# Kernel optimization log

Hardware: AMD Instinct MI355X
Metric: run time of the kernel (lower is better)

Reference implementation:

```python
import jax, jax.numpy as jnp
import numpy as np

B, L, H, E = 8, 1024, 8, 64
S, D = 1024, 64


def fp(x):
    # power-norm with p=2: norm(x) * x^2 / norm(x^2)
    norm = jnp.sqrt(jnp.sum(x * x, axis=-1, keepdims=True))
    px = x * x  # x^p, p=2
    pnorm = jnp.sqrt(jnp.sum(px * px, axis=-1, keepdims=True))
    return norm * px / pnorm


def phi_p(x):
    return fp(jax.nn.relu(x))


def setup_inputs() -> dict:
    key = jax.random.key(0)
    kq, kk, kv = jax.random.split(key, 3)
    queries = jax.random.normal(kq, (B, L, H, E), dtype=jnp.float32)
    keys = jax.random.normal(kk, (B, S, H, E), dtype=jnp.float32)
    values = jax.random.normal(kv, (B, S, H, D), dtype=jnp.float32)
    # all-False mask: masked_fill(-inf) + fp() would NaN otherwise (see notes)
    attn_mask = jnp.zeros((B, 1, L, S), dtype=bool)
    return {"queries": queries, "keys": keys, "values": values, "attn_mask": attn_mask}


def reference(queries, keys, values, attn_mask):
    qt = phi_p(queries)              # [B,L,H,E]
    kt = phi_p(keys)                 # [B,S,H,E]
    scores = jnp.einsum('blhe,bshe->bhls', qt, kt)  # [B,H,L,S]
    scores = jnp.where(attn_mask, -jnp.inf, scores)  # mask_flag=True path
    # NB: original computes scale = 1/sqrt(E) but never applies it.
    A = jax.nn.softmax(fp(scores), axis=-1)  # dropout is identity at eval
    V = jnp.einsum('bhls,bshd->blhd', A, values)  # [B,L,H,D]
    return V
```

## Files before the change

### kernel.cpp

```cpp
#include <hip/hip_runtime.h>
#include <hip/hip_bf16.h>


#define B_ 8
#define L_ 1024
#define H_ 8
#define E_ 64
#define S_ 1024
#define D_ 64
#define BH_ 64

typedef _Float16 f16_t;
typedef _Float16 f16x8 __attribute__((ext_vector_type(8)));
typedef _Float16 f16x4v __attribute__((ext_vector_type(4)));
typedef float f32x4 __attribute__((ext_vector_type(4)));
typedef unsigned u32x4 __attribute__((ext_vector_type(4)));

#define MFMA16F(a, b, c) __builtin_amdgcn_mfma_f32_16x16x32_f16(a, b, c, 0, 0, 0)
#define GLDS16(g, l)                                                        \
  __builtin_amdgcn_global_load_lds(                                         \
      (const __attribute__((address_space(1))) void*)(g),                   \
      (__attribute__((address_space(3))) void*)(l), 16, 0, 0)

#if __has_builtin(__builtin_amdgcn_exp2f)
#define EXP2(x) __builtin_amdgcn_exp2f(x)
#else
#define EXP2(x) exp2f(x)
#endif

static __device__ __forceinline__ unsigned pkh(float a, float b) {
  return __builtin_bit_cast(unsigned, __builtin_amdgcn_cvt_pkrtz(a, b));
}

static __device__ __forceinline__ void pl32_swap(unsigned& x, unsigned& y) {
#if __has_builtin(__builtin_amdgcn_permlane32_swap)
  auto r = __builtin_amdgcn_permlane32_swap(x, y, false, false);
  x = r[0];
  y = r[1];
#else
  unsigned xs = __shfl_xor((int)x, 32, 64), ys = __shfl_xor((int)y, 32, 64);
  bool hi = (threadIdx.x & 32) != 0;
  unsigned nx = hi ? ys : x;
  unsigned ny = hi ? y : xs;
  x = nx;
  y = ny;
#endif
}

static __device__ __forceinline__ void pl16_swap(unsigned& x, unsigned& y) {
#if __has_builtin(__builtin_amdgcn_permlane16_swap)
  auto r = __builtin_amdgcn_permlane16_swap(x, y, false, false);
  x = r[0];
  y = r[1];
#else
  unsigned xs = __shfl_xor((int)x, 16, 64), ys = __shfl_xor((int)y, 16, 64);
  bool odd = (threadIdx.x & 16) != 0;
  unsigned nx = odd ? ys : x;
  unsigned ny = odd ? y : xs;
  x = nx;
  y = ny;
#endif
}

__global__ __launch_bounds__(256) void prep_kernel(
    const float* __restrict__ q, const float* __restrict__ k,
    const float* __restrict__ v, f16_t* __restrict__ qf,
    f16_t* __restrict__ kf, f16_t* __restrict__ vt) {
  __shared__ float tile[32][68];
  int bid = blockIdx.x;
  if (bid < 8192) {
    int row = bid * 16 + (threadIdx.x >> 4);
    int p = threadIdx.x & 15;
    const float* src;
    f16_t* dst;
    int r = row;
    if (r < B_ * L_ * H_) { src = q; dst = qf; }
    else { r -= B_ * L_ * H_; src = k; dst = kf; }
    int b = r >> 13;
    int l = (r >> 3) & 1023;
    int h = r & 7;
    float4 x = ((const float4*)(src + (size_t)r * 64))[p];
    float s0 = fmaxf(x.x, 0.f) * fmaxf(x.x, 0.f);
    float s1 = fmaxf(x.y, 0.f) * fmaxf(x.y, 0.f);
    float s2 = fmaxf(x.z, 0.f) * fmaxf(x.z, 0.f);
    float s3 = fmaxf(x.w, 0.f) * fmaxf(x.w, 0.f);
    float sum2 = (s0 + s1) + (s2 + s3);
    float sum4 = fmaf(s0, s0, s1 * s1) + fmaf(s2, s2, s3 * s3);
#pragma unroll
    for (int off = 1; off < 16; off <<= 1) {
      sum2 += __shfl_xor(sum2, off, 64);
      sum4 += __shfl_xor(sum4, off, 64);
    }
    float sc = (sum4 > 0.f) ? sqrtf(sum2 / sum4) : 0.f;
    f16x4v o = {(f16_t)(sc * s0), (f16_t)(sc * s1), (f16_t)(sc * s2),
                (f16_t)(sc * s3)};
    int c = p >> 1, e = (p & 1) * 4;
    int col = (((c ^ (l & 7)) << 3) | e);
    *(f16x4v*)(dst + ((size_t)(b * H_ + h) * 1024 + l) * 64 + col) = o;
  } else {
    int vb = bid - 8192;
    int bh = vb >> 5;
    int st = vb & 31;
    int b = bh >> 3, h = bh & 7;
    int t = threadIdx.x;
    int sl = t >> 3, dp = t & 7;
    const float* src =
        v + (((size_t)(b * S_ + st * 32 + sl) * H_ + h) * D_) + dp * 8;
    float4 f0 = ((const float4*)src)[0];
    float4 f1 = ((const float4*)src)[1];
    *(float4*)&tile[sl][dp * 8] = f0;
    *(float4*)&tile[sl][dp * 8 + 4] = f1;
    __syncthreads();
    int d = t >> 2, sc = t & 3;
    f16_t tmp[8];
#pragma unroll
    for (int j = 0; j < 8; ++j) tmp[j] = (f16_t)tile[sc * 8 + j][d];
    f16_t* dst =
        vt + (((size_t)bh * 32 + st) * 64 + d) * 32 + (sc ^ ((d >> 1) & 3)) * 8;
    *(uint4*)dst = *(const uint4*)tmp;
  }
}

__global__ __launch_bounds__(512, 4) void attn_kernel(
    const f16_t* __restrict__ qf, const f16_t* __restrict__ kf,
    const f16_t* __restrict__ vt, float* __restrict__ out) {
  __shared__ __align__(16) f16_t k_t[2][2][2048];
  __shared__ __align__(16) f16_t v_t[2][2][2048];
  __shared__ __align__(16) float mrg[4][64][34];

  int bh = blockIdx.x & 63;
  int qb = blockIdx.x >> 6;
  int b = bh >> 3, h = bh & 7;
  int tid = threadIdx.x;
  int wave = tid >> 6, lane = tid & 63;
  int wv = wave & 3, sh = wave >> 2;
  int g = lane >> 4, n = lane & 15;

  const f16_t* qf_b = qf + ((size_t)bh * L_ + qb * 128) * 64;
  const f16_t* kf_b = kf + (size_t)bh * S_ * 64 + (size_t)sh * 16 * 2048;
  const f16_t* vt_b = vt + (size_t)bh * 32 * 2048 + (size_t)sh * 16 * 2048;

  int arow = wv * 32 + n;
  int qoff0 = arow * 64 + ((g ^ (n & 7)) << 3);
  int qoff1 = qoff0 + 16 * 64;
  f16x8 qa0_0 = *(const f16x8*)(qf_b + qoff0);
  f16x8 qa1_0 = *(const f16x8*)(qf_b + (qoff0 ^ 32));
  f16x8 qa0_1 = *(const f16x8*)(qf_b + qoff1);
  f16x8 qa1_1 = *(const f16x8*)(qf_b + (qoff1 ^ 32));

  int koff = n * 64 + ((g ^ (n & 7)) << 3);
  int voff = n * 32 + ((g ^ ((n >> 1) & 3)) << 3);
  int so = (tid & 255) * 8;

  const f32x4 fzero = {0.f, 0.f, 0.f, 0.f};
  f32x4 acc2_0 = fzero, acc4_0 = fzero, mx_0 = fzero;
  f32x4 acc2_1 = fzero, acc4_1 = fzero, mx_1 = fzero;

  GLDS16(kf_b + so, &k_t[sh][0][so]);
  for (int t = 0; t < 16; ++t) {
    __syncthreads();
    if (t < 15)
      GLDS16(kf_b + (t + 1) * 2048 + so, &k_t[sh][(t + 1) & 1][so]);
    const f16_t* kt = k_t[sh][t & 1];
    f16x8 b00 = *(const f16x8*)(kt + koff);
    f16x8 b01 = *(const f16x8*)(kt + (koff ^ 32));
    f16x8 b10 = *(const f16x8*)(kt + koff + 1024);
    f16x8 b11 = *(const f16x8*)(kt + (koff ^ 32) + 1024);
    f32x4 sc0_0 = MFMA16F(b00, qa0_0, fzero);
    sc0_0 = MFMA16F(b01, qa1_0, sc0_0);
    f32x4 sc1_0 = MFMA16F(b10, qa0_0, fzero);
    sc1_0 = MFMA16F(b11, qa1_0, sc1_0);
    f32x4 sc0_1 = MFMA16F(b00, qa0_1, fzero);
    sc0_1 = MFMA16F(b01, qa1_1, sc0_1);
    f32x4 sc1_1 = MFMA16F(b10, qa0_1, fzero);
    sc1_1 = MFMA16F(b11, qa1_1, sc1_1);
    f32x4 t0 = sc0_0 * sc0_0, t1 = sc1_0 * sc1_0;
    acc2_0 += t0 + t1;
    acc4_0 += t0 * t0;
    acc4_0 += t1 * t1;
    mx_0 = __builtin_elementwise_max(mx_0, __builtin_elementwise_max(t0, t1));
    f32x4 u0 = sc0_1 * sc0_1, u1 = sc1_1 * sc1_1;
    acc2_1 += u0 + u1;
    acc4_1 += u0 * u0;
    acc4_1 += u1 * u1;
    mx_1 = __builtin_elementwise_max(mx_1, __builtin_elementwise_max(u0, u1));
  }
  GLDS16(kf_b + so, &k_t[sh][0][so]);
  GLDS16(vt_b + so, &v_t[sh][0][so]);

  float a2_0 = (acc2_0[0] + acc2_0[1]) + (acc2_0[2] + acc2_0[3]);
  float a4_0 = (acc4_0[0] + acc4_0[1]) + (acc4_0[2] + acc4_0[3]);
  float m2_0 = fmaxf(fmaxf(mx_0[0], mx_0[1]), fmaxf(mx_0[2], mx_0[3]));
  float a2_1 = (acc2_1[0] + acc2_1[1]) + (acc2_1[2] + acc2_1[3]);
  float a4_1 = (acc4_1[0] + acc4_1[1]) + (acc4_1[2] + acc4_1[3]);
  float m2_1 = fmaxf(fmaxf(mx_1[0], mx_1[1]), fmaxf(mx_1[2], mx_1[3]));
  a2_0 += __shfl_xor(a2_0, 16, 64);
  a4_0 += __shfl_xor(a4_0, 16, 64);
  m2_0 = fmaxf(m2_0, __shfl_xor(m2_0, 16, 64));
  a2_1 += __shfl_xor(a2_1, 16, 64);
  a4_1 += __shfl_xor(a4_1, 16, 64);
  m2_1 = fmaxf(m2_1, __shfl_xor(m2_1, 16, 64));
  a2_0 += __shfl_xor(a2_0, 32, 64);
  a4_0 += __shfl_xor(a4_0, 32, 64);
  m2_0 = fmaxf(m2_0, __shfl_xor(m2_0, 32, 64));
  a2_1 += __shfl_xor(a2_1, 32, 64);
  a4_1 += __shfl_xor(a4_1, 32, 64);
  m2_1 = fmaxf(m2_1, __shfl_xor(m2_1, 32, 64));

  {
    float* sm = &mrg[0][0][0] + ((size_t)(wave * 64 + lane)) * 6;
    sm[0] = a2_0; sm[1] = a4_0; sm[2] = m2_0;
    sm[3] = a2_1; sm[4] = a4_1; sm[5] = m2_1;
  }
  __syncthreads();
  {
    const float* sp = &mrg[0][0][0] + ((size_t)((wave ^ 4) * 64 + lane)) * 6;
    a2_0 += sp[0]; a4_0 += sp[1]; m2_0 = fmaxf(m2_0, sp[2]);
    a2_1 += sp[3]; a4_1 += sp[4]; m2_1 = fmaxf(m2_1, sp[5]);
  }
  const float LOG2E = 1.44269504f;
  float c2_0 = (a4_0 > 0.f) ? (sqrtf(a2_0 / a4_0) * LOG2E) : 0.f;
  float cm2_0 = c2_0 * m2_0;
  float c2_1 = (a4_1 > 0.f) ? (sqrtf(a2_1 / a4_1) * LOG2E) : 0.f;
  float cm2_1 = c2_1 * m2_1;

  f32x4 pv0[4], pv1[4];
#pragma unroll
  for (int dg = 0; dg < 4; ++dg) { pv0[dg] = fzero; pv1[dg] = fzero; }
  f32x4 denv0 = fzero, denv1 = fzero;

  for (int t = 0; t < 16; ++t) {
    __syncthreads();
    if (t < 15) {
      int go = (t + 1) * 2048 + so;
      int bs = (t + 1) & 1;
      GLDS16(kf_b + go, &k_t[sh][bs][so]);
      GLDS16(vt_b + go, &v_t[sh][bs][so]);
    }
    const f16_t* kt = k_t[sh][t & 1];
    const f16_t* vl = v_t[sh][t & 1];
    f16x8 vb[4];
#pragma unroll
    for (int dg = 0; dg < 4; ++dg)
      vb[dg] = *(const f16x8*)(vl + voff + dg * 512);
    f16x8 b00 = *(const f16x8*)(kt + koff);
    f16x8 b01 = *(const f16x8*)(kt + (koff ^ 32));
    f16x8 b10 = *(const f16x8*)(kt + koff + 1024);
    f16x8 b11 = *(const f16x8*)(kt + (koff ^ 32) + 1024);
    f32x4 sc0_0 = MFMA16F(b00, qa0_0, fzero);
    sc0_0 = MFMA16F(b01, qa1_0, sc0_0);
    f32x4 sc1_0 = MFMA16F(b10, qa0_0, fzero);
    sc1_0 = MFMA16F(b11, qa1_0, sc1_0);
    f32x4 sc0_1 = MFMA16F(b00, qa0_1, fzero);
    sc0_1 = MFMA16F(b01, qa1_1, sc0_1);
    f32x4 sc1_1 = MFMA16F(b10, qa0_1, fzero);
    sc1_1 = MFMA16F(b11, qa1_1, sc1_1);
    f32x4 e0 = sc0_0 * sc0_0 * c2_0 - cm2_0;
    f32x4 e1 = sc1_0 * sc1_0 * c2_0 - cm2_0;
    f32x4 w0, w1;
#pragma unroll
    for (int r = 0; r < 4; ++r) { w0[r] = EXP2(e0[r]); w1[r] = EXP2(e1[r]); }
    denv0 += w0 + w1;
    unsigned X0 = pkh(w0[0], w0[1]), X1 = pkh(w0[2], w0[3]);
    unsigned Y0 = pkh(w1[0], w1[1]), Y1 = pkh(w1[2], w1[3]);
    pl32_swap(X0, Y0);
    pl16_swap(X0, Y0);
    pl32_swap(X1, Y1);
    pl16_swap(X1, Y1);
    u32x4 fu0 = {X0, X1, Y0, Y1};
    f16x8 wa0 = __builtin_bit_cast(f16x8, fu0);
    f32x4 f0v = sc0_1 * sc0_1 * c2_1 - cm2_1;
    f32x4 f1v = sc1_1 * sc1_1 * c2_1 - cm2_1;
    f32x4 z0, z1;
#pragma unroll
    for (int r = 0; r < 4; ++r) { z0[r] = EXP2(f0v[r]); z1[r] = EXP2(f1v[r]); }
    denv1 += z0 + z1;
    unsigned P0 = pkh(z0[0], z0[1]), P1 = pkh(z0[2], z0[3]);
    unsigned Q0 = pkh(z1[0], z1[1]), Q1 = pkh(z1[2], z1[3]);
    pl32_swap(P0, Q0);
    pl16_swap(P0, Q0);
    pl32_swap(P1, Q1);
    pl16_swap(P1, Q1);
    u32x4 fu1 = {P0, P1, Q0, Q1};
    f16x8 wa1 = __builtin_bit_cast(f16x8, fu1);
#pragma unroll
    for (int dg = 0; dg < 4; ++dg) {
      pv0[dg] = MFMA16F(wa0, vb[dg], pv0[dg]);
      pv1[dg] = MFMA16F(wa1, vb[dg], pv1[dg]);
    }
  }

  float den0 = (denv0[0] + denv0[1]) + (denv0[2] + denv0[3]);
  den0 += __shfl_xor(den0, 16, 64);
  den0 += __shfl_xor(den0, 32, 64);
  float den1 = (denv1[0] + denv1[1]) + (denv1[2] + denv1[3]);
  den1 += __shfl_xor(den1, 16, 64);
  den1 += __shfl_xor(den1, 32, 64);

  __syncthreads();
  if (sh == 1) {
    float* mp = &mrg[wv][lane][0];
#pragma unroll
    for (int dg = 0; dg < 4; ++dg)
#pragma unroll
      for (int r = 0; r < 4; ++r) {
        mp[dg * 4 + r] = pv0[dg][r];
        mp[16 + dg * 4 + r] = pv1[dg][r];
      }
    mp[32] = den0;
    mp[33] = den1;
  }
  __syncthreads();
  if (sh == 0) {
    const float* mp = &mrg[wv][lane][0];
#pragma unroll
    for (int dg = 0; dg < 4; ++dg)
#pragma unroll
      for (int r = 0; r < 4; ++r) {
        pv0[dg][r] += mp[dg * 4 + r];
        pv1[dg][r] += mp[16 + dg * 4 + r];
      }
    den0 += mp[32];
    den1 += mp[33];
#pragma unroll
    for (int r = 0; r < 4; ++r) {
      float dr0 = __shfl(den0, g * 4 + r, 64);
      float inv0 = 1.f / dr0;
      int l0 = qb * 128 + wv * 32 + g * 4 + r;
      float* op0 = out + (((size_t)b * L_ + l0) * H_ + h) * D_;
#pragma unroll
      for (int dg = 0; dg < 4; ++dg) op0[dg * 16 + n] = pv0[dg][r] * inv0;
      float dr1 = __shfl(den1, g * 4 + r, 64);
      float inv1 = 1.f / dr1;
      int l1 = l0 + 16;
      float* op1 = out + (((size_t)b * L_ + l1) * H_ + h) * D_;
#pragma unroll
      for (int dg = 0; dg < 4; ++dg) op1[dg * 16 + n] = pv1[dg][r] * inv1;
    }
  }
}

extern "C" void kernel_launch(void* const* d_in, const int* in_sizes, int n_in,
                              void* d_out, int out_size, void* d_ws, size_t ws_size,
                              hipStream_t stream) {
  const float* q = (const float*)d_in[0];
  const float* k = (const float*)d_in[1];
  const float* v = (const float*)d_in[2];
  float* out = (float*)d_out;

  const size_t NE = (size_t)B_ * L_ * H_ * E_;
  f16_t* qf = (f16_t*)d_ws;
  f16_t* kf = qf + NE;
  f16_t* vt = kf + NE;

  prep_kernel<<<8192 + 2048, 256, 0, stream>>>(q, k, v, qf, kf, vt);
  attn_kernel<<<BH_ * (L_ / 128), 512, 0, stream>>>(qf, kf, vt, out);
}
```

Before: 147.3 us.

## Split key sequence across four wave groups per block with tree merge

Doubles the block to 1024 threads so four wave groups each process a quarter of the key/value sequence, instead of two halves. This raises per-block parallelism and shortens each group's serial loop over key tiles. In exchange it needs a 4-way merge of the norm statistics and a two-stage tree reduction of partial PV accumulators through a shared buffer that reuses the K/V tile space, with an XOR swizzle. The tighter launch bounds may squeeze registers and cause spills.

```diff
diff --git a/kernel.cpp b/kernel.cpp
--- a/kernel.cpp
+++ b/kernel.cpp
@@ -121,12 +121,14 @@
   }
 }
 
-__global__ __launch_bounds__(512, 4) void attn_kernel(
+__global__ __launch_bounds__(1024, 8) void attn_kernel(
     const f16_t* __restrict__ qf, const f16_t* __restrict__ kf,
     const f16_t* __restrict__ vt, float* __restrict__ out) {
-  __shared__ __align__(16) f16_t k_t[2][2][2048];
-  __shared__ __align__(16) f16_t v_t[2][2][2048];
-  __shared__ __align__(16) float mrg[4][64][34];
+  __shared__ __align__(16) unsigned char smem[71680];
+  f16_t (*k_t)[2][2048] = reinterpret_cast<f16_t(*)[2][2048]>(smem);
+  f16_t (*v_t)[2][2048] = reinterpret_cast<f16_t(*)[2][2048]>(smem + 32768);
+  float* stats = reinterpret_cast<float*>(smem + 65536);
+  float* mrg = reinterpret_cast<float*>(smem);
 
   int bh = blockIdx.x & 63;
   int qb = blockIdx.x >> 6;
@@ -137,8 +139,8 @@
   int g = lane >> 4, n = lane & 15;
 
   const f16_t* qf_b = qf + ((size_t)bh * L_ + qb * 128) * 64;
-  const f16_t* kf_b = kf + (size_t)bh * S_ * 64 + (size_t)sh * 16 * 2048;
-  const f16_t* vt_b = vt + (size_t)bh * 32 * 2048 + (size_t)sh * 16 * 2048;
+  const f16_t* kf_q = kf + (size_t)bh * S_ * 64 + (size_t)sh * 8 * 2048;
+  const f16_t* vt_q = vt + (size_t)bh * 32 * 2048 + (size_t)sh * 8 * 2048;
 
   int arow = wv * 32 + n;
   int qoff0 = arow * 64 + ((g ^ (n & 7)) << 3);
@@ -156,11 +158,11 @@
   f32x4 acc2_0 = fzero, acc4_0 = fzero, mx_0 = fzero;
   f32x4 acc2_1 = fzero, acc4_1 = fzero, mx_1 = fzero;
 
-  GLDS16(kf_b + so, &k_t[sh][0][so]);
-  for (int t = 0; t < 16; ++t) {
+  GLDS16(kf_q + so, &k_t[sh][0][so]);
+  for (int t = 0; t < 8; ++t) {
     __syncthreads();
-    if (t < 15)
-      GLDS16(kf_b + (t + 1) * 2048 + so, &k_t[sh][(t + 1) & 1][so]);
+    if (t < 7)
+      GLDS16(kf_q + (t + 1) * 2048 + so, &k_t[sh][(t + 1) & 1][so]);
     const f16_t* kt = k_t[sh][t & 1];
     f16x8 b00 = *(const f16x8*)(kt + koff);
     f16x8 b01 = *(const f16x8*)(kt + (koff ^ 32));
@@ -185,8 +187,8 @@
     acc4_1 += u1 * u1;
     mx_1 = __builtin_elementwise_max(mx_1, __builtin_elementwise_max(u0, u1));
   }
-  GLDS16(kf_b + so, &k_t[sh][0][so]);
-  GLDS16(vt_b + so, &v_t[sh][0][so]);
+  GLDS16(kf_q + so, &k_t[sh][0][so]);
+  GLDS16(vt_q + so, &v_t[sh][0][so]);
 
   float a2_0 = (acc2_0[0] + acc2_0[1]) + (acc2_0[2] + acc2_0[3]);
   float a4_0 = (acc4_0[0] + acc4_0[1]) + (acc4_0[2] + acc4_0[3]);
@@ -207,35 +209,38 @@
   a4_1 += __shfl_xor(a4_1, 32, 64);
   m2_1 = fmaxf(m2_1, __shfl_xor(m2_1, 32, 64));
 
-  {
-    float* sm = &mrg[0][0][0] + ((size_t)(wave * 64 + lane)) * 6;
-    sm[0] = a2_0; sm[1] = a4_0; sm[2] = m2_0;
-    sm[3] = a2_1; sm[4] = a4_1; sm[5] = m2_1;
-  }
-  __syncthreads();
-  {
-    const float* sp = &mrg[0][0][0] + ((size_t)((wave ^ 4) * 64 + lane)) * 6;
-    a2_0 += sp[0]; a4_0 += sp[1]; m2_0 = fmaxf(m2_0, sp[2]);
-    a2_1 += sp[3]; a4_1 += sp[4]; m2_1 = fmaxf(m2_1, sp[5]);
+  if (g == 0) {
+    float* sp = stats + ((size_t)(wave * 16 + n)) * 6;
+    sp[0] = a2_0; sp[1] = a4_0; sp[2] = m2_0;
+    sp[3] = a2_1; sp[4] = a4_1; sp[5] = m2_1;
+  }
+  __syncthreads();
+  float A2_0 = 0.f, A4_0 = 0.f, M2_0 = 0.f;
+  float A2_1 = 0.f, A4_1 = 0.f, M2_1 = 0.f;
+#pragma unroll
+  for (int qq = 0; qq < 4; ++qq) {
+    const float* sp = stats + ((size_t)((qq * 4 + wv) * 16 + n)) * 6;
+    A2_0 += sp[0]; A4_0 += sp[1]; M2_0 = fmaxf(M2_0, sp[2]);
+    A2_1 += sp[3]; A4_1 += sp[4]; M2_1 = fmaxf(M2_1, sp[5]);
   }
   const float LOG2E = 1.44269504f;
-  float c2_0 = (a4_0 > 0.f) ? (sqrtf(a2_0 / a4_0) * LOG2E) : 0.f;
-  float cm2_0 = c2_0 * m2_0;
-  float c2_1 = (a4_1 > 0.f) ? (sqrtf(a2_1 / a4_1) * LOG2E) : 0.f;
-  float cm2_1 = c2_1 * m2_1;
+  float c2_0 = (A4_0 > 0.f) ? (sqrtf(A2_0 / A4_0) * LOG2E) : 0.f;
+  float cm2_0 = c2_0 * M2_0;
+  float c2_1 = (A4_1 > 0.f) ? (sqrtf(A2_1 / A4_1) * LOG2E) : 0.f;
+  float cm2_1 = c2_1 * M2_1;
 
   f32x4 pv0[4], pv1[4];
 #pragma unroll
   for (int dg = 0; dg < 4; ++dg) { pv0[dg] = fzero; pv1[dg] = fzero; }
   f32x4 denv0 = fzero, denv1 = fzero;
 
-  for (int t = 0; t < 16; ++t) {
+  for (int t = 0; t < 8; ++t) {
     __syncthreads();
-    if (t < 15) {
+    if (t < 7) {
       int go = (t + 1) * 2048 + so;
       int bs = (t + 1) & 1;
-      GLDS16(kf_b + go, &k_t[sh][bs][so]);
-      GLDS16(vt_b + go, &v_t[sh][bs][so]);
+      GLDS16(kf_q + go, &k_t[sh][bs][so]);
+      GLDS16(vt_q + go, &v_t[sh][bs][so]);
     }
     const f16_t* kt = k_t[sh][t & 1];
     const f16_t* vl = v_t[sh][t & 1];
@@ -297,31 +302,58 @@
   den1 += __shfl_xor(den1, 16, 64);
   den1 += __shfl_xor(den1, 32, 64);
 
+  int cs = lane & 7;
+  __syncthreads();
+  if (sh >= 2) {
+    float* mp = mrg + (((size_t)((sh - 2) * 4 + wv) * 64 + lane)) * 32;
+#pragma unroll
+    for (int j = 0; j < 4; ++j) {
+      ((f32x4*)mp)[j ^ cs] = pv0[j];
+      ((f32x4*)mp)[(j + 4) ^ cs] = pv1[j];
+    }
+    if (g == 0) {
+      float* dp = stats + ((size_t)((sh - 2) * 4 + wv) * 16 + n) * 2;
+      dp[0] = den0;
+      dp[1] = den1;
+    }
+  }
+  __syncthreads();
+  if (sh < 2) {
+    const float* mp = mrg + (((size_t)(sh * 4 + wv) * 64 + lane)) * 32;
+#pragma unroll
+    for (int j = 0; j < 4; ++j) {
+      pv0[j] += ((const f32x4*)mp)[j ^ cs];
+      pv1[j] += ((const f32x4*)mp)[(j + 4) ^ cs];
+    }
+    const float* dp = stats + ((size_t)(sh * 4 + wv) * 16 + n) * 2;
+    den0 += dp[0];
+    den1 += dp[1];
+  }
   __syncthreads();
   if (sh == 1) {
-    float* mp = &mrg[wv][lane][0];
-#pragma unroll
-    for (int dg = 0; dg < 4; ++dg)
-#pragma unroll
-      for (int r = 0; r < 4; ++r) {
-        mp[dg * 4 + r] = pv0[dg][r];
-        mp[16 + dg * 4 + r] = pv1[dg][r];
-      }
-    mp[32] = den0;
-    mp[33] = den1;
+    float* mp = mrg + (((size_t)wv * 64 + lane)) * 32;
+#pragma unroll
+    for (int j = 0; j < 4; ++j) {
+      ((f32x4*)mp)[j ^ cs] = pv0[j];
+      ((f32x4*)mp)[(j + 4) ^ cs] = pv1[j];
+    }
+    if (g == 0) {
+      float* dp = stats + 256 + ((size_t)wv * 16 + n) * 2;
+      dp[0] = den0;
+      dp[1] = den1;
+    }
   }
   __syncthreads();
   if (sh == 0) {
-    const float* mp = &mrg[wv][lane][0];
-#pragma unroll
-    for (int dg = 0; dg < 4; ++dg)
-#pragma unroll
-      for (int r = 0; r < 4; ++r) {
-        pv0[dg][r] += mp[dg * 4 + r];
-        pv1[dg][r] += mp[16 + dg * 4 + r];
-      }
-    den0 += mp[32];
-    den1 += mp[33];
+    const float* mp = mrg + (((size_t)wv * 64 + lane)) * 32;
+#pragma unroll
+    for (int j = 0; j < 4; ++j) {
+      pv0[j] += ((const f32x4*)mp)[j ^ cs];
+      pv1[j] += ((const f32x4*)mp)[(j + 4) ^ cs];
+    }
+    const float* dp = stats + 256 + ((size_t)wv * 16 + n) * 2;
+    den0 += dp[0];
+    den1 += dp[1];
 #pragma unroll
     for (int r = 0; r < 4; ++r) {
       float dr0 = __shfl(den0, g * 4 + r, 64);
@@ -354,5 +386,5 @@
   f16_t* vt = kf + NE;
 
   prep_kernel<<<8192 + 2048, 256, 0, stream>>>(q, k, v, qf, kf, vt);
-  attn_kernel<<<BH_ * (L_ / 128), 512, 0, stream>>>(qf, kf, vt, out);
-}
+  attn_kernel<<<BH_ * (L_ / 128), 1024, 0, stream>>>(qf, kf, vt, out);
+}
```

Measured after the change: 388.9 us. 2.64x slower.
